# Kernel tuning notes

Hardware: AMD Instinct MI355X
Metric: run time of the kernel (lower is better)

The kernel has to match this reference:

```python
import jax, jax.numpy as jnp
import numpy as np

L, B, E, H = 512, 32, 1024, 16
NEG = -1e9  # finite stand-in for masked_fill(-inf); avoids NaNs if a row were fully masked


def setup_inputs() -> dict:
    key = jax.random.key(0)
    ks = jax.random.split(key, 6)
    s_in = (2.0 / (3 * E + E)) ** 0.5   # xavier-ish scale for in_proj
    s_out = (2.0 / (E + E)) ** 0.5
    return {
        "query": jax.random.normal(ks[0], (L, B, E), jnp.float32),
        "key": jax.random.normal(ks[1], (L, B, E), jnp.float32),
        "value": jax.random.normal(ks[2], (L, B, E), jnp.float32),
        "attn_mask": jax.random.randint(ks[3], (B, L, L), 0, 2).astype(jnp.bool_),
        "in_proj_weight": jax.random.normal(ks[4], (3 * E, E), jnp.float32) * s_in,
        "in_proj_bias": jnp.zeros((3 * E,), jnp.float32),
        "out_proj_weight": jax.random.normal(ks[5], (E, E), jnp.float32) * s_out,
        "out_proj_bias": jnp.zeros((E,), jnp.float32),
        "num_heads": H,
    }


def reference(query, key, value, attn_mask, in_proj_weight, in_proj_bias,
              out_proj_weight, out_proj_bias, num_heads):
    Lq, Bz, Em = query.shape
    hd = Em // num_heads
    Wq, Wk, Wv = jnp.split(in_proj_weight, 3, axis=0)
    bq, bk, bv = jnp.split(in_proj_bias, 3, axis=0)
    # in-projection: x @ W^T + b  (torch F.linear convention)
    q = query @ Wq.T + bq
    k = key @ Wk.T + bk
    v = value @ Wv.T + bv
    # [L, B, E] -> [B*H, L, hd], batch-major (b*H + h) per torch view semantics
    def split_heads(x):
        return x.reshape(x.shape[0], Bz * num_heads, hd).transpose(1, 0, 2)
    q, k, v = split_heads(q), split_heads(k), split_heads(v)
    q = q / jnp.sqrt(jnp.asarray(hd, q.dtype))
    # scores: [B*H, Lq, Lk]
    attn = jnp.einsum('bqd,bkd->bqk', q, k)
    # mask broadcast to heads: [B, L, L] -> [B*H, L, L] with index b*H + h
    mask_mh = jnp.repeat(attn_mask, num_heads, axis=0)
    # original: scatter zeros where masked, then masked_fill(-inf) inside
    # multi_head_positional_attention; net effect = mask -> -inf before softmax
    attn = jnp.where(mask_mh, NEG, attn)
    p = jax.nn.softmax(attn, axis=-1)
    out = jnp.einsum('bqk,bkd->bqd', p, v)        # [B*H, Lq, hd]
    out = out.transpose(1, 0, 2).reshape(Lq, Bz, Em)
    out = out @ out_proj_weight.T + out_proj_bias  # [L, B, E]
    return out
```

## Files before the change

### kernel.cpp

```cpp
#include <hip/hip_runtime.h>
#include <hip/hip_bf16.h>
#include <stdint.h>

#define LSEQ 512
#define BATCH 32
#define EMB 1024
#define NHEAD 16
#define HDIM 64
#define TOK (LSEQ*BATCH)
#define BHTOT (BATCH*NHEAD)

typedef __attribute__((ext_vector_type(8))) short short8;
typedef __attribute__((ext_vector_type(4))) short short4v;
typedef __attribute__((ext_vector_type(4))) float f32x4;

__device__ __forceinline__ short f2bf(float f) {
  __hip_bfloat16 h = __float2bfloat16(f);
  union { __hip_bfloat16 h; short s; } u; u.h = h;
  return u.s;
}

__device__ __forceinline__ short8 cvt8(f32x4 x0, f32x4 x1) {
  short8 o;
  o[0] = f2bf(x0[0]); o[1] = f2bf(x0[1]); o[2] = f2bf(x0[2]); o[3] = f2bf(x0[3]);
  o[4] = f2bf(x1[0]); o[5] = f2bf(x1[1]); o[6] = f2bf(x1[2]); o[7] = f2bf(x1[3]);
  return o;
}

#if defined(__has_builtin)
#if __has_builtin(__builtin_amdgcn_global_load_lds)
#define HAVE_GLL 1
#endif
#endif

__device__ __forceinline__ void gload_lds16(const void* g, void* l) {
#ifdef HAVE_GLL
  __builtin_amdgcn_global_load_lds((const __attribute__((address_space(1))) void*)g,
                                   (__attribute__((address_space(3))) void*)l, 16, 0, 0);
#else
  *(short8*)l = *(const short8*)g;
#endif
}

#define WAIT_VM8  do { asm volatile("s_waitcnt vmcnt(8)" ::: "memory"); __builtin_amdgcn_sched_barrier(0); } while (0)
#define WAIT_VM4  do { asm volatile("s_waitcnt vmcnt(4)" ::: "memory"); __builtin_amdgcn_sched_barrier(0); } while (0)
#define WAIT_VM0  do { asm volatile("s_waitcnt vmcnt(0)" ::: "memory"); __builtin_amdgcn_sched_barrier(0); } while (0)
#define WAIT_LGKM0 do { asm volatile("s_waitcnt lgkmcnt(0)" ::: "memory"); __builtin_amdgcn_sched_barrier(0); } while (0)
#define BAR() __builtin_amdgcn_s_barrier()

__global__ __launch_bounds__(256) void castx_kernel(const float* __restrict__ xq,
                                                    const float* __restrict__ xk,
                                                    const float* __restrict__ xv,
                                                    short* __restrict__ xb)
{
  const size_t i = blockIdx.x * 256 + threadIdx.x;
  #pragma unroll
  for (int it = 0; it < 6; ++it) {
    const float* src = (it < 2) ? xq : (it < 4) ? xk : xv;
    size_t p = i + (size_t)it * 1048576;
    size_t local = p - (size_t)(it >> 1) * 2097152;
    f32x4 x0 = __builtin_nontemporal_load((const f32x4*)src + 2 * local);
    f32x4 x1 = __builtin_nontemporal_load((const f32x4*)src + 2 * local + 1);
    __builtin_nontemporal_store(cvt8(x0, x1), (short8*)xb + p);
  }
}

__global__ __launch_bounds__(256) void prep2_kernel(const float* __restrict__ W,
                                                    const float* __restrict__ Wo,
                                                    const float* __restrict__ bias,
                                                    short* __restrict__ Wb, short* __restrict__ Wob,
                                                    float* __restrict__ biasp,
                                                    const int* __restrict__ mask,
                                                    uint32_t* __restrict__ mb)
{
  const int i = blockIdx.x * 256 + threadIdx.x;
  if (i < 786432) {
    f32x4 v = ((const f32x4*)W)[i];
    int row = i >> 8;
    float s = (row < 1024) ? 0.125f : 1.0f;
    short4v o;
    o[0] = f2bf(v[0]*s); o[1] = f2bf(v[1]*s); o[2] = f2bf(v[2]*s); o[3] = f2bf(v[3]*s);
    ((short4v*)Wb)[i] = o;
  } else {
    int j = i - 786432;
    f32x4 v = ((const f32x4*)Wo)[j];
    short4v o;
    o[0] = f2bf(v[0]); o[1] = f2bf(v[1]); o[2] = f2bf(v[2]); o[3] = f2bf(v[3]);
    ((short4v*)Wob)[j] = o;
  }
  if (i < 768) {
    f32x4 v = ((const f32x4*)bias)[i];
    float s = (i < 256) ? 0.125f : 1.0f;
    f32x4 o = {v[0]*s, v[1]*s, v[2]*s, v[3]*s};
    ((f32x4*)biasp)[i] = o;
  }
  {
    int w = i >> 6;
    int lane = threadIdx.x & 63;
    int src_idx = ((lane & 3) << 4) | (lane >> 2);
    const int* src = mask + ((size_t)w << 9);
    uint32_t* dst = mb + w * 16;
    #pragma unroll
    for (int c = 0; c < 8; ++c) {
      int v = src[c * 64 + src_idx];
      unsigned long long m = __ballot(v != 0);
      if (lane == 0) dst[c*2]     = (uint32_t)m;
      if (lane == 1) dst[c*2 + 1] = (uint32_t)(m >> 32);
    }
  }
}


#define FRAG_READ(AsX, BsX)                                           \
    short8 af[4], bfr[4];                                             \
    _Pragma("unroll")                                                 \
    for (int mi = 0; mi < 4; ++mi) {                                  \
      int row = wm + mi * 16 + l15;                                   \
      int cs = l4 ^ ((row >> 1) & 3);                                 \
      af[mi] = *(const short8*)&AsX[row * 32 + cs * 8];               \
    }                                                                 \
    _Pragma("unroll")                                                 \
    for (int ni = 0; ni < 4; ++ni) {                                  \
      int row = wn + ni * 16 + l15;                                   \
      int cs = l4 ^ ((row >> 1) & 3);                                 \
      bfr[ni] = *(const short8*)&BsX[row * 32 + cs * 8];              \
    }

#define DO_MFMA()                                                     \
    _Pragma("unroll")                                                 \
    for (int mi = 0; mi < 4; ++mi)                                    \
      _Pragma("unroll")                                               \
      for (int ni = 0; ni < 4; ++ni)                                  \
        acc[mi][ni] = __builtin_amdgcn_mfma_f32_16x16x32_bf16(af[mi], bfr[ni], acc[mi][ni], 0, 0, 0)

#define ISSUE(AsX, BsX, koff)                                         \
    _Pragma("unroll")                                                 \
    for (int jj = 0; jj < 2; ++jj) {                                  \
      gload_lds16(aSrc[jj] + (koff), &AsX[sDst[jj]]);                 \
      gload_lds16(bSrc[jj] + (koff), &BsX[sDst[jj]]);                 \
    }

#define GSTEP_I(AsX, BsX, WAITM, koff)                                \
  { WAITM; BAR();                                                     \
    FRAG_READ(AsX, BsX);                                              \
    WAIT_LGKM0; BAR();                                                \
    ISSUE(AsX, BsX, koff);                                            \
    DO_MFMA(); }

#define GSTEP_N(AsX, BsX, WAITM)                                      \
  { WAITM; BAR();                                                     \
    FRAG_READ(AsX, BsX);                                              \
    WAIT_LGKM0; BAR();                                                \
    DO_MFMA(); }

#define STAGE_COORDS(Abase, Bbase)                                    \
  const short* aSrc[2]; const short* bSrc[2]; int sDst[2];            \
  _Pragma("unroll")                                                   \
  for (int jj = 0; jj < 2; ++jj) {                                    \
    int ch = tid + jj * 256;                                          \
    int row = ch >> 2, cl = ch & 3;                                   \
    int cs = cl ^ ((row >> 1) & 3);                                   \
    aSrc[jj] = (Abase) + (size_t)(m0 + row) * 1024 + cs * 8;          \
    bSrc[jj] = (Bbase) + (size_t)(n0 + row) * 1024 + cs * 8;          \
    sDst[jj] = ch * 8;                                                \
  }

#define PIPE_BODY()                                                   \
  ISSUE(As0, Bs0, 0); ISSUE(As1, Bs1, 32); ISSUE(As2, Bs2, 64);       \
  for (int i = 0; i < 9; ++i) {                                       \
    const int s = 3 * i;                                              \
    GSTEP_I(As0, Bs0, WAIT_VM8, (s + 3) * 32);                        \
    GSTEP_I(As1, Bs1, WAIT_VM8, (s + 4) * 32);                        \
    GSTEP_I(As2, Bs2, WAIT_VM8, (s + 5) * 32);                        \
  }                                                                   \
  GSTEP_I(As0, Bs0, WAIT_VM8, 30 * 32);                               \
  GSTEP_I(As1, Bs1, WAIT_VM8, 31 * 32);                               \
  GSTEP_N(As2, Bs2, WAIT_VM8);                                        \
  GSTEP_N(As0, Bs0, WAIT_VM4);                                        \
  GSTEP_N(As1, Bs1, WAIT_VM0);

__launch_bounds__(256, 3)
__global__ void proj_gemm(const short* __restrict__ xb, const short* __restrict__ W,
                          const float* __restrict__ biasp,
                          short* __restrict__ qh, short* __restrict__ kh,
                          short* __restrict__ vh)
{
  int z = blockIdx.z;
  const short* A = xb + (size_t)z * TOK * EMB;
  short* C       = (z == 0) ? qh : (z == 1) ? kh : vh;
  const short* B = W + (size_t)z * 1024 * 1024;
  const float* bp = biasp + z * 1024;

  int flat = blockIdx.y * 8 + blockIdx.x;
  int X = flat & 7, s0 = flat >> 3;
  int m0 = (X * 16 + (s0 >> 3)) * 128;
  int n0 = (s0 & 7) * 128;

  __shared__ alignas(16) short As0[128 * 32];
  __shared__ alignas(16) short As1[128 * 32];
  __shared__ alignas(16) short As2[128 * 32];
  __shared__ alignas(16) short Bs0[128 * 32];
  __shared__ alignas(16) short Bs1[128 * 32];
  __shared__ alignas(16) short Bs2[128 * 32];

  const int tid = threadIdx.x, lane = tid & 63;
  const int w = tid >> 6;
  const int wm = (w >> 1) * 64, wn = (w & 1) * 64;
  const int l15 = lane & 15, l4 = lane >> 4;

  STAGE_COORDS(A, B);

  f32x4 acc[4][4];
  #pragma unroll
  for (int mi = 0; mi < 4; ++mi)
    #pragma unroll
    for (int ni = 0; ni < 4; ++ni) acc[mi][ni] = f32x4{0.f, 0.f, 0.f, 0.f};

  PIPE_BODY();

  #pragma unroll
  for (int ni = 0; ni < 4; ++ni) {
    int gcol = n0 + wn + ni * 16 + l15;
    float bv = bp[gcol];
    int h = gcol >> 6, d = gcol & 63;
    #pragma unroll
    for (int mi = 0; mi < 4; ++mi) {
      int growb = m0 + wm + mi * 16 + l4 * 4;
      #pragma unroll
      for (int r = 0; r < 4; ++r) {
        int grow = growb + r;
        int lsq = grow >> 5, bb = grow & 31;
        C[((size_t)((bb * NHEAD + h) * LSEQ + lsq)) * HDIM + d] = f2bf(acc[mi][ni][r] + bv);
      }
    }
  }
}

__launch_bounds__(256, 3)
__global__ void out_gemm(const short* __restrict__ Ab, const short* __restrict__ W,
                         const float* __restrict__ bo, float* __restrict__ out)
{
  int flat = blockIdx.y * 8 + blockIdx.x;
  int X = flat & 7, s0 = flat >> 3;
  int m0 = (X * 16 + (s0 >> 3)) * 128;
  int n0 = (s0 & 7) * 128;

  __shared__ alignas(16) short As0[128 * 32];
  __shared__ alignas(16) short As1[128 * 32];
  __shared__ alignas(16) short As2[128 * 32];
  __shared__ alignas(16) short Bs0[128 * 32];
  __shared__ alignas(16) short Bs1[128 * 32];
  __shared__ alignas(16) short Bs2[128 * 32];

  const int tid = threadIdx.x, lane = tid & 63;
  const int w = tid >> 6;
  const int wm = (w >> 1) * 64, wn = (w & 1) * 64;
  const int l15 = lane & 15, l4 = lane >> 4;

  STAGE_COORDS(Ab, W);

  f32x4 acc[4][4];
  #pragma unroll
  for (int mi = 0; mi < 4; ++mi)
    #pragma unroll
    for (int ni = 0; ni < 4; ++ni) acc[mi][ni] = f32x4{0.f, 0.f, 0.f, 0.f};

  ISSUE(As0, Bs0, 0); ISSUE(As1, Bs1, 32); ISSUE(As2, Bs2, 64);
  for (int i = 0; i < 9; ++i) {
    const int s = 3 * i;
    GSTEP_I(As0, Bs0, WAIT_VM8, (s + 3) * 32);
    GSTEP_I(As1, Bs1, WAIT_VM8, (s + 4) * 32);
    GSTEP_I(As2, Bs2, WAIT_VM8, (s + 5) * 32);
  }
  GSTEP_I(As0, Bs0, WAIT_VM8, 30 * 32);
  GSTEP_I(As1, Bs1, WAIT_VM8, 31 * 32);
  GSTEP_N(As2, Bs2, WAIT_VM8);
  GSTEP_N(As0, Bs0, WAIT_VM4);
  GSTEP_N(As1, Bs1, WAIT_VM0);

  #pragma unroll
  for (int ni = 0; ni < 4; ++ni) {
    int gcol = n0 + wn + ni * 16 + l15;
    float bv = bo[gcol];
    #pragma unroll
    for (int mi = 0; mi < 4; ++mi) {
      int growb = m0 + wm + mi * 16 + l4 * 4;
      #pragma unroll
      for (int r = 0; r < 4; ++r)
        out[(size_t)(growb + r) * 1024 + gcol] = acc[mi][ni][r] + bv;
    }
  }
}

__launch_bounds__(256, 4)
__global__ void attn_kernel(const short* __restrict__ qh, const short* __restrict__ kh,
                            const short* __restrict__ vh, const uint32_t* __restrict__ mb,
                            short* __restrict__ ao)
{
  int flat = blockIdx.y * 8 + blockIdx.x;
  int X = flat & 7, s = flat >> 3;
  int bh = X * 64 + (s >> 2);
  int qblk = s & 3;
  int b = bh >> 4, h = bh & 15;
  int q0 = qblk * 128;

  const int tid = threadIdx.x, lane = tid & 63, w = tid >> 6;
  const int l15 = lane & 15, l4 = lane >> 4;

  __shared__ alignas(16) short Ks[64 * 64];
  __shared__ alignas(16) short Vt[64 * 72];
  __shared__ alignas(16) short Ps[4 * 32 * 72];
  __shared__ uint32_t Mw[128 * 2];

  const size_t bhoff = (size_t)bh * (LSEQ * HDIM);

  short8 aq[2][2];
  #pragma unroll
  for (int m = 0; m < 2; ++m) {
    int qrow = q0 + w * 32 + m * 16 + l15;
    const short* qp = qh + bhoff + (size_t)qrow * HDIM + l4 * 8;
    aq[m][0] = *(const short8*)qp;
    aq[m][1] = *(const short8*)(qp + 32);
  }

  f32x4 oacc[2][4];
  float l_part[2][4];
  #pragma unroll
  for (int m = 0; m < 2; ++m) {
    #pragma unroll
    for (int n = 0; n < 4; ++n) oacc[m][n] = f32x4{0.f, 0.f, 0.f, 0.f};
    #pragma unroll
    for (int r = 0; r < 4; ++r) l_part[m][r] = 0.f;
  }

  for (int kt = 0; kt < 8; ++kt) {
    __syncthreads();
    #pragma unroll
    for (int jj = 0; jj < 2; ++jj) {
      int ch = tid + jj * 256;
      int row = ch >> 3, cl = ch & 7;
      int cg = cl ^ (row & 7);
      const short* g = kh + bhoff + (size_t)(kt * 64 + row) * HDIM + cg * 8;
      gload_lds16(g, &Ks[ch * 8]);
    }
    #pragma unroll
    for (int jj = 0; jj < 2; ++jj) {
      int c = tid + jj * 256;
      int kv = c & 63, d0 = (c >> 6) * 8;
      const short* g = vh + bhoff + (size_t)(kt * 64 + kv) * HDIM + d0;
      short8 vv = *(const short8*)g;
      #pragma unroll
      for (int j = 0; j < 8; ++j) Vt[(d0 + j) * 72 + kv] = vv[j];
    }
    {
      int qr = tid >> 1, wd = tid & 1;
      Mw[qr * 2 + wd] = mb[((size_t)b * LSEQ + q0 + qr) * 16 + kt * 2 + wd];
    }
    __syncthreads();

    f32x4 sa[2][4];
    #pragma unroll
    for (int m = 0; m < 2; ++m)
      #pragma unroll
      for (int n = 0; n < 4; ++n) sa[m][n] = f32x4{0.f, 0.f, 0.f, 0.f};
    #pragma unroll
    for (int ss = 0; ss < 2; ++ss) {
      #pragma unroll
      for (int n = 0; n < 4; ++n) {
        int row = n * 16 + l15;
        int cs = (ss * 4 + l4) ^ (row & 7);
        short8 bk = *(const short8*)&Ks[row * 64 + cs * 8];
        #pragma unroll
        for (int m = 0; m < 2; ++m)
          sa[m][n] = __builtin_amdgcn_mfma_f32_16x16x32_bf16(aq[m][ss], bk, sa[m][n], 0, 0, 0);
      }
    }

    #pragma unroll
    for (int m = 0; m < 2; ++m) {
      #pragma unroll
      for (int r = 0; r < 4; ++r) {
        int qr = w * 32 + m * 16 + l4 * 4 + r;
        uint32_t wsel = Mw[qr * 2 + (l15 >> 3)];
        uint32_t nib = wsel >> ((l15 & 7) * 4);
        float p0 = (nib & 1u) ? 0.f : __expf(sa[m][0][r]);
        float p1 = (nib & 2u) ? 0.f : __expf(sa[m][1][r]);
        float p2 = (nib & 4u) ? 0.f : __expf(sa[m][2][r]);
        float p3 = (nib & 8u) ? 0.f : __expf(sa[m][3][r]);
        l_part[m][r] += (p0 + p1) + (p2 + p3);
        short* pp = &Ps[w * 2304 + (m * 16 + l4 * 4 + r) * 72];
        pp[0 * 16 + l15] = f2bf(p0);
        pp[1 * 16 + l15] = f2bf(p1);
        pp[2 * 16 + l15] = f2bf(p2);
        pp[3 * 16 + l15] = f2bf(p3);
      }
    }

    #pragma unroll
    for (int ss = 0; ss < 2; ++ss) {
      short8 pa[2];
      #pragma unroll
      for (int m = 0; m < 2; ++m)
        pa[m] = *(const short8*)&Ps[w * 2304 + (m * 16 + l15) * 72 + ss * 32 + l4 * 8];
      #pragma unroll
      for (int n = 0; n < 4; ++n) {
        short8 bv = *(const short8*)&Vt[(n * 16 + l15) * 72 + ss * 32 + l4 * 8];
        #pragma unroll
        for (int m = 0; m < 2; ++m)
          oacc[m][n] = __builtin_amdgcn_mfma_f32_16x16x32_bf16(pa[m], bv, oacc[m][n], 0, 0, 0);
      }
    }
  }

  #pragma unroll
  for (int m = 0; m < 2; ++m) {
    #pragma unroll
    for (int r = 0; r < 4; ++r) {
      float l = l_part[m][r];
      #pragma unroll
      for (int off = 1; off < 16; off <<= 1) l += __shfl_xor(l, off, 64);
      float inv = 1.0f / fmaxf(l, 1e-30f);
      int qrow = q0 + w * 32 + m * 16 + l4 * 4 + r;
      size_t tbase = ((size_t)qrow * BATCH + b) * EMB + h * HDIM;
      #pragma unroll
      for (int n = 0; n < 4; ++n)
        ao[tbase + n * 16 + l15] = f2bf(oacc[m][n][r] * inv);
    }
  }
}

extern "C" void kernel_launch(void* const* d_in, const int* in_sizes, int n_in,
                              void* d_out, int out_size, void* d_ws, size_t ws_size,
                              hipStream_t stream) {
  const float* q_in = (const float*)d_in[0];
  const float* k_in = (const float*)d_in[1];
  const float* v_in = (const float*)d_in[2];
  const int*   mask = (const int*)d_in[3];
  const float* Wp   = (const float*)d_in[4];
  const float* bp   = (const float*)d_in[5];
  const float* Wo   = (const float*)d_in[6];
  const float* bo   = (const float*)d_in[7];

  char* ws = (char*)d_ws;
  short* Wb    = (short*)ws;    ws += (size_t)3072 * 1024 * 2;
  short* Wob   = (short*)ws;    ws += (size_t)1024 * 1024 * 2;
  float* biasp = (float*)ws;    ws += (size_t)3072 * 4;
  uint32_t* mb = (uint32_t*)ws; ws += (size_t)BATCH * LSEQ * 16 * 4;
  short* qh    = (short*)ws;    ws += (size_t)TOK * EMB * 2;
  short* kh    = (short*)ws;    ws += (size_t)TOK * EMB * 2;
  short* vh    = (short*)ws;    ws += (size_t)TOK * EMB * 2;
  short* xb    = (short*)ws;    ws += (size_t)3 * TOK * EMB * 2;
  short* ao    = xb;

  castx_kernel<<<4096, 256, 0, stream>>>(q_in, k_in, v_in, xb);
  prep2_kernel<<<4096, 256, 0, stream>>>(Wp, Wo, bp, Wb, Wob, biasp, mask, mb);
  proj_gemm<<<dim3(8, 128, 3), 256, 0, stream>>>(xb, Wb, biasp, qh, kh, vh);
  attn_kernel<<<dim3(8, 256), 256, 0, stream>>>(qh, kh, vh, mb, ao);
  out_gemm<<<dim3(8, 128), 256, 0, stream>>>(ao, Wob, bo, (float*)d_out);
}
```

Before: 317.5 us.

## Restructure GEMM pipeline to process two K-slices per barrier with four LDS buffers

The projection and output GEMMs move from a 3-stage LDS ring that handles one 32-wide K slice per barrier pair to a 4-buffer scheme that handles two K slices (64 wide) per step. This halves the number of barriers and waitcnt syncs per K loop and gives more MFMA work between synchronisations. In exchange LDS use per block rises from 48KB to 64KB and fragment registers double, so launch bounds drop from 3 to 2 blocks per CU, which lowers occupancy.

Measured after the change: 327.0 us. 1.03x slower.

```diff
diff --git a/kernel.cpp b/kernel.cpp
--- a/kernel.cpp
+++ b/kernel.cpp
@@ -43,7 +43,6 @@
 }
 
 #define WAIT_VM8  do { asm volatile("s_waitcnt vmcnt(8)" ::: "memory"); __builtin_amdgcn_sched_barrier(0); } while (0)
-#define WAIT_VM4  do { asm volatile("s_waitcnt vmcnt(4)" ::: "memory"); __builtin_amdgcn_sched_barrier(0); } while (0)
 #define WAIT_VM0  do { asm volatile("s_waitcnt vmcnt(0)" ::: "memory"); __builtin_amdgcn_sched_barrier(0); } while (0)
 #define WAIT_LGKM0 do { asm volatile("s_waitcnt lgkmcnt(0)" ::: "memory"); __builtin_amdgcn_sched_barrier(0); } while (0)
 #define BAR() __builtin_amdgcn_s_barrier()
@@ -111,8 +110,7 @@
 }
 
 
-#define FRAG_READ(AsX, BsX)                                           \
-    short8 af[4], bfr[4];                                             \
+#define FRAG_READ2(AsX, BsX, af, bfr)                                 \
     _Pragma("unroll")                                                 \
     for (int mi = 0; mi < 4; ++mi) {                                  \
       int row = wm + mi * 16 + l15;                                   \
@@ -126,7 +124,7 @@
       bfr[ni] = *(const short8*)&BsX[row * 32 + cs * 8];              \
     }
 
-#define DO_MFMA()                                                     \
+#define MFMA16(af, bfr)                                               \
     _Pragma("unroll")                                                 \
     for (int mi = 0; mi < 4; ++mi)                                    \
       _Pragma("unroll")                                               \
@@ -140,18 +138,22 @@
       gload_lds16(bSrc[jj] + (koff), &BsX[sDst[jj]]);                 \
     }
 
-#define GSTEP_I(AsX, BsX, WAITM, koff)                                \
+#define GSTEP2_I(Aa, Ba, Ab, Bb, koff)                                \
+  { WAIT_VM8; BAR();                                                  \
+    short8 afa[4], bfa[4], afb[4], bfb[4];                            \
+    FRAG_READ2(Aa, Ba, afa, bfa);                                     \
+    FRAG_READ2(Ab, Bb, afb, bfb);                                     \
+    WAIT_LGKM0; BAR();                                                \
+    ISSUE(Aa, Ba, (koff)); ISSUE(Ab, Bb, (koff) + 32);                \
+    MFMA16(afa, bfa); MFMA16(afb, bfb); }
+
+#define GSTEP2_N(Aa, Ba, Ab, Bb, WAITM)                               \
   { WAITM; BAR();                                                     \
-    FRAG_READ(AsX, BsX);                                              \
+    short8 afa[4], bfa[4], afb[4], bfb[4];                            \
+    FRAG_READ2(Aa, Ba, afa, bfa);                                     \
+    FRAG_READ2(Ab, Bb, afb, bfb);                                     \
     WAIT_LGKM0; BAR();                                                \
-    ISSUE(AsX, BsX, koff);                                            \
-    DO_MFMA(); }
-
-#define GSTEP_N(AsX, BsX, WAITM)                                      \
-  { WAITM; BAR();                                                     \
-    FRAG_READ(AsX, BsX);                                              \
-    WAIT_LGKM0; BAR();                                                \
-    DO_MFMA(); }
+    MFMA16(afa, bfa); MFMA16(afb, bfb); }
 
 #define STAGE_COORDS(Abase, Bbase)                                    \
   const short* aSrc[2]; const short* bSrc[2]; int sDst[2];            \
@@ -165,21 +167,17 @@
     sDst[jj] = ch * 8;                                                \
   }
 
-#define PIPE_BODY()                                                   \
-  ISSUE(As0, Bs0, 0); ISSUE(As1, Bs1, 32); ISSUE(As2, Bs2, 64);       \
-  for (int i = 0; i < 9; ++i) {                                       \
-    const int s = 3 * i;                                              \
-    GSTEP_I(As0, Bs0, WAIT_VM8, (s + 3) * 32);                        \
-    GSTEP_I(As1, Bs1, WAIT_VM8, (s + 4) * 32);                        \
-    GSTEP_I(As2, Bs2, WAIT_VM8, (s + 5) * 32);                        \
+#define PIPE2_BODY()                                                  \
+  ISSUE(As0, Bs0, 0);  ISSUE(As1, Bs1, 32);                           \
+  ISSUE(As2, Bs2, 64); ISSUE(As3, Bs3, 96);                           \
+  for (int i = 0; i < 7; ++i) {                                       \
+    GSTEP2_I(As0, Bs0, As1, Bs1, (4 * i + 4) * 32);                   \
+    GSTEP2_I(As2, Bs2, As3, Bs3, (4 * i + 6) * 32);                   \
   }                                                                   \
-  GSTEP_I(As0, Bs0, WAIT_VM8, 30 * 32);                               \
-  GSTEP_I(As1, Bs1, WAIT_VM8, 31 * 32);                               \
-  GSTEP_N(As2, Bs2, WAIT_VM8);                                        \
-  GSTEP_N(As0, Bs0, WAIT_VM4);                                        \
-  GSTEP_N(As1, Bs1, WAIT_VM0);
-
-__launch_bounds__(256, 3)
+  GSTEP2_N(As0, Bs0, As1, Bs1, WAIT_VM8);                             \
+  GSTEP2_N(As2, Bs2, As3, Bs3, WAIT_VM0);
+
+__launch_bounds__(256, 2)
 __global__ void proj_gemm(const short* __restrict__ xb, const short* __restrict__ W,
                           const float* __restrict__ biasp,
                           short* __restrict__ qh, short* __restrict__ kh,
@@ -199,9 +197,11 @@
   __shared__ alignas(16) short As0[128 * 32];
   __shared__ alignas(16) short As1[128 * 32];
   __shared__ alignas(16) short As2[128 * 32];
+  __shared__ alignas(16) short As3[128 * 32];
   __shared__ alignas(16) short Bs0[128 * 32];
   __shared__ alignas(16) short Bs1[128 * 32];
   __shared__ alignas(16) short Bs2[128 * 32];
+  __shared__ alignas(16) short Bs3[128 * 32];
 
   const int tid = threadIdx.x, lane = tid & 63;
   const int w = tid >> 6;
@@ -216,7 +216,7 @@
     #pragma unroll
     for (int ni = 0; ni < 4; ++ni) acc[mi][ni] = f32x4{0.f, 0.f, 0.f, 0.f};
 
-  PIPE_BODY();
+  PIPE2_BODY();
 
   #pragma unroll
   for (int ni = 0; ni < 4; ++ni) {
@@ -236,7 +236,7 @@
   }
 }
 
-__launch_bounds__(256, 3)
+__launch_bounds__(256, 2)
 __global__ void out_gemm(const short* __restrict__ Ab, const short* __restrict__ W,
                          const float* __restrict__ bo, float* __restrict__ out)
 {
@@ -248,9 +248,11 @@
   __shared__ alignas(16) short As0[128 * 32];
   __shared__ alignas(16) short As1[128 * 32];
   __shared__ alignas(16) short As2[128 * 32];
+  __shared__ alignas(16) short As3[128 * 32];
   __shared__ alignas(16) short Bs0[128 * 32];
   __shared__ alignas(16) short Bs1[128 * 32];
   __shared__ alignas(16) short Bs2[128 * 32];
+  __shared__ alignas(16) short Bs3[128 * 32];
 
   const int tid = threadIdx.x, lane = tid & 63;
   const int w = tid >> 6;
@@ -265,18 +267,7 @@
     #pragma unroll
     for (int ni = 0; ni < 4; ++ni) acc[mi][ni] = f32x4{0.f, 0.f, 0.f, 0.f};
 
-  ISSUE(As0, Bs0, 0); ISSUE(As1, Bs1, 32); ISSUE(As2, Bs2, 64);
-  for (int i = 0; i < 9; ++i) {
-    const int s = 3 * i;
-    GSTEP_I(As0, Bs0, WAIT_VM8, (s + 3) * 32);
-    GSTEP_I(As1, Bs1, WAIT_VM8, (s + 4) * 32);
-    GSTEP_I(As2, Bs2, WAIT_VM8, (s + 5) * 32);
-  }
-  GSTEP_I(As0, Bs0, WAIT_VM8, 30 * 32);
-  GSTEP_I(As1, Bs1, WAIT_VM8, 31 * 32);
-  GSTEP_N(As2, Bs2, WAIT_VM8);
-  GSTEP_N(As0, Bs0, WAIT_VM4);
-  GSTEP_N(As1, Bs1, WAIT_VM0);
+  PIPE2_BODY();
 
   #pragma unroll
   for (int ni = 0; ni < 4; ++ni) {
```

## Stage GEMM and attention epilogues through LDS for coalesced vector stores

Applied to the files above, without the earlier changes.

Merges each kernel's shared buffers into one array and reuses it after the main loop as a per-wave transpose scratch. Accumulator fragments are written to LDS with a padded stride of 65 floats, then read back row-wise so each lane emits contiguous 16-byte global stores. This replaces the scattered 2-byte bf16 and 4-byte fp32 stores in the projection, attention and output kernels. Out_gemm's hand-unrolled pipeline is also swapped for the shared PIPE_BODY macro. The cost is an extra barrier and a round trip through LDS in every epilogue.

After: 345.6 us. 1.09x slower.

```diff
diff --git a/kernel.cpp b/kernel.cpp
--- a/kernel.cpp
+++ b/kernel.cpp
@@ -196,12 +196,13 @@
   int m0 = (X * 16 + (s0 >> 3)) * 128;
   int n0 = (s0 & 7) * 128;
 
-  __shared__ alignas(16) short As0[128 * 32];
-  __shared__ alignas(16) short As1[128 * 32];
-  __shared__ alignas(16) short As2[128 * 32];
-  __shared__ alignas(16) short Bs0[128 * 32];
-  __shared__ alignas(16) short Bs1[128 * 32];
-  __shared__ alignas(16) short Bs2[128 * 32];
+  __shared__ alignas(16) short SM[24576];
+  short* const As0 = SM;
+  short* const As1 = SM + 4096;
+  short* const As2 = SM + 8192;
+  short* const Bs0 = SM + 12288;
+  short* const Bs1 = SM + 16384;
+  short* const Bs2 = SM + 20480;
 
   const int tid = threadIdx.x, lane = tid & 63;
   const int w = tid >> 6;
@@ -218,19 +219,36 @@
 
   PIPE_BODY();
 
-  #pragma unroll
-  for (int ni = 0; ni < 4; ++ni) {
-    int gcol = n0 + wn + ni * 16 + l15;
-    float bv = bp[gcol];
-    int h = gcol >> 6, d = gcol & 63;
-    #pragma unroll
-    for (int mi = 0; mi < 4; ++mi) {
-      int growb = m0 + wm + mi * 16 + l4 * 4;
-      #pragma unroll
-      for (int r = 0; r < 4; ++r) {
-        int grow = growb + r;
-        int lsq = grow >> 5, bb = grow & 31;
-        C[((size_t)((bb * NHEAD + h) * LSEQ + lsq)) * HDIM + d] = f2bf(acc[mi][ni][r] + bv);
+  __syncthreads();
+  {
+    float* T = (float*)&SM[w * 6144];
+    const int hh = (n0 + wn) >> 6;
+    float bv[4];
+    #pragma unroll
+    for (int ni = 0; ni < 4; ++ni) bv[ni] = bp[n0 + wn + ni * 16 + l15];
+    #pragma unroll
+    for (int p = 0; p < 2; ++p) {
+      WAIT_LGKM0;
+      #pragma unroll
+      for (int mi2 = 0; mi2 < 2; ++mi2) {
+        int mi = p * 2 + mi2;
+        #pragma unroll
+        for (int ni = 0; ni < 4; ++ni)
+          #pragma unroll
+          for (int r = 0; r < 4; ++r)
+            T[(mi2 * 16 + l4 * 4 + r) * 65 + ni * 16 + l15] = acc[mi][ni][r] + bv[ni];
+      }
+      WAIT_LGKM0;
+      int rl = lane & 31, half = lane >> 5;
+      int grow = m0 + wm + p * 32 + rl;
+      int lsq = grow >> 5, bb = grow & 31;
+      short* dst = C + ((size_t)((bb * NHEAD + hh) * LSEQ + lsq)) * HDIM + half * 32;
+      const float* src = T + rl * 65 + half * 32;
+      #pragma unroll
+      for (int c = 0; c < 4; ++c) {
+        f32x4 x0 = { src[c*8+0], src[c*8+1], src[c*8+2], src[c*8+3] };
+        f32x4 x1 = { src[c*8+4], src[c*8+5], src[c*8+6], src[c*8+7] };
+        *(short8*)(dst + c * 8) = cvt8(x0, x1);
       }
     }
   }
@@ -245,12 +263,13 @@
   int m0 = (X * 16 + (s0 >> 3)) * 128;
   int n0 = (s0 & 7) * 128;
 
-  __shared__ alignas(16) short As0[128 * 32];
-  __shared__ alignas(16) short As1[128 * 32];
-  __shared__ alignas(16) short As2[128 * 32];
-  __shared__ alignas(16) short Bs0[128 * 32];
-  __shared__ alignas(16) short Bs1[128 * 32];
-  __shared__ alignas(16) short Bs2[128 * 32];
+  __shared__ alignas(16) short SM[24576];
+  short* const As0 = SM;
+  short* const As1 = SM + 4096;
+  short* const As2 = SM + 8192;
+  short* const Bs0 = SM + 12288;
+  short* const Bs1 = SM + 16384;
+  short* const Bs2 = SM + 20480;
 
   const int tid = threadIdx.x, lane = tid & 63;
   const int w = tid >> 6;
@@ -265,29 +284,36 @@
     #pragma unroll
     for (int ni = 0; ni < 4; ++ni) acc[mi][ni] = f32x4{0.f, 0.f, 0.f, 0.f};
 
-  ISSUE(As0, Bs0, 0); ISSUE(As1, Bs1, 32); ISSUE(As2, Bs2, 64);
-  for (int i = 0; i < 9; ++i) {
-    const int s = 3 * i;
-    GSTEP_I(As0, Bs0, WAIT_VM8, (s + 3) * 32);
-    GSTEP_I(As1, Bs1, WAIT_VM8, (s + 4) * 32);
-    GSTEP_I(As2, Bs2, WAIT_VM8, (s + 5) * 32);
-  }
-  GSTEP_I(As0, Bs0, WAIT_VM8, 30 * 32);
-  GSTEP_I(As1, Bs1, WAIT_VM8, 31 * 32);
-  GSTEP_N(As2, Bs2, WAIT_VM8);
-  GSTEP_N(As0, Bs0, WAIT_VM4);
-  GSTEP_N(As1, Bs1, WAIT_VM0);
-
-  #pragma unroll
-  for (int ni = 0; ni < 4; ++ni) {
-    int gcol = n0 + wn + ni * 16 + l15;
-    float bv = bo[gcol];
-    #pragma unroll
-    for (int mi = 0; mi < 4; ++mi) {
-      int growb = m0 + wm + mi * 16 + l4 * 4;
-      #pragma unroll
-      for (int r = 0; r < 4; ++r)
-        out[(size_t)(growb + r) * 1024 + gcol] = acc[mi][ni][r] + bv;
+  PIPE_BODY();
+
+  __syncthreads();
+  {
+    float* T = (float*)&SM[w * 6144];
+    float bv[4];
+    #pragma unroll
+    for (int ni = 0; ni < 4; ++ni) bv[ni] = bo[n0 + wn + ni * 16 + l15];
+    #pragma unroll
+    for (int p = 0; p < 2; ++p) {
+      WAIT_LGKM0;
+      #pragma unroll
+      for (int mi2 = 0; mi2 < 2; ++mi2) {
+        int mi = p * 2 + mi2;
+        #pragma unroll
+        for (int ni = 0; ni < 4; ++ni)
+          #pragma unroll
+          for (int r = 0; r < 4; ++r)
+            T[(mi2 * 16 + l4 * 4 + r) * 65 + ni * 16 + l15] = acc[mi][ni][r] + bv[ni];
+      }
+      WAIT_LGKM0;
+      int rl = lane & 31, half = lane >> 5;
+      int grow = m0 + wm + p * 32 + rl;
+      float* dst = out + (size_t)grow * 1024 + n0 + wn + half * 32;
+      const float* src = T + rl * 65 + half * 32;
+      #pragma unroll
+      for (int c = 0; c < 8; ++c) {
+        f32x4 x = { src[c*4+0], src[c*4+1], src[c*4+2], src[c*4+3] };
+        *(f32x4*)(dst + c * 4) = x;
+      }
     }
   }
 }
@@ -307,10 +333,11 @@
   const int tid = threadIdx.x, lane = tid & 63, w = tid >> 6;
   const int l15 = lane & 15, l4 = lane >> 4;
 
-  __shared__ alignas(16) short Ks[64 * 64];
-  __shared__ alignas(16) short Vt[64 * 72];
-  __shared__ alignas(16) short Ps[4 * 32 * 72];
-  __shared__ uint32_t Mw[128 * 2];
+  __shared__ alignas(16) short SM[18944];
+  short* const Ks = SM;
+  short* const Vt = SM + 4096;
+  short* const Ps = SM + 8704;
+  uint32_t* const Mw = (uint32_t*)(SM + 17920);
 
   const size_t bhoff = (size_t)bh * (LSEQ * HDIM);
 
@@ -412,6 +439,7 @@
     }
   }
 
+  float inv_[2][4];
   #pragma unroll
   for (int m = 0; m < 2; ++m) {
     #pragma unroll
@@ -419,12 +447,29 @@
       float l = l_part[m][r];
       #pragma unroll
       for (int off = 1; off < 16; off <<= 1) l += __shfl_xor(l, off, 64);
-      float inv = 1.0f / fmaxf(l, 1e-30f);
-      int qrow = q0 + w * 32 + m * 16 + l4 * 4 + r;
-      size_t tbase = ((size_t)qrow * BATCH + b) * EMB + h * HDIM;
+      inv_[m][r] = 1.0f / fmaxf(l, 1e-30f);
+    }
+  }
+  __syncthreads();
+  {
+    float* T = (float*)&SM[w * 4160];
+    #pragma unroll
+    for (int m = 0; m < 2; ++m)
       #pragma unroll
       for (int n = 0; n < 4; ++n)
-        ao[tbase + n * 16 + l15] = f2bf(oacc[m][n][r] * inv);
+        #pragma unroll
+        for (int r = 0; r < 4; ++r)
+          T[(m * 16 + l4 * 4 + r) * 65 + n * 16 + l15] = oacc[m][n][r] * inv_[m][r];
+    WAIT_LGKM0;
+    int rl = lane & 31, half = lane >> 5;
+    int qrow = q0 + w * 32 + rl;
+    short* dst = ao + ((size_t)qrow * BATCH + b) * EMB + h * HDIM + half * 32;
+    const float* src = T + rl * 65 + half * 32;
+    #pragma unroll
+    for (int c = 0; c < 4; ++c) {
+      f32x4 x0 = { src[c*8+0], src[c*8+1], src[c*8+2], src[c*8+3] };
+      f32x4 x1 = { src[c*8+4], src[c*8+5], src[c*8+6], src[c*8+7] };
+      *(short8*)(dst + c * 8) = cvt8(x0, x1);
     }
   }
 }
```
